# Kernel tuning notes

Hardware: AMD Instinct MI355X
Metric: run time of the kernel (lower is better)

## Reference

```python
import jax, jax.numpy as jnp
import numpy as np

N = 50000      # nodes
DIM = 128      # feature dim
H = 4          # heads
C = DIM // H   # per-head channels
E = 800000     # edges (before self-loops)
LRELU_SLOPE = 0.2
LN_EPS = 1e-5


def setup_inputs() -> dict:
    key = jax.random.key(0)
    ks = jax.random.split(key, 12)
    def p(k, shape, scale=0.05):
        return jax.random.normal(k, shape, jnp.float32) * scale
    return {
        "x": jax.random.normal(ks[0], (N, DIM), jnp.float32),
        "edge_index": jax.random.randint(ks[1], (2, E), 0, N),
        "W1": p(ks[2], (DIM, DIM)), "b1": jnp.zeros((DIM,), jnp.float32),
        "att_src1": p(ks[3], (H, C)), "att_dst1": p(ks[4], (H, C)),
        "W2": p(ks[5], (DIM, DIM)), "b2": jnp.zeros((DIM,), jnp.float32),
        "att_src2": p(ks[6], (H, C)), "att_dst2": p(ks[7], (H, C)),
        "gate_W": p(ks[8], (2 * DIM, 2)), "gate_b": jnp.zeros((2,), jnp.float32),
        "ln_gamma": jnp.ones((DIM,), jnp.float32), "ln_beta": jnp.zeros((DIM,), jnp.float32),
    }


def _gat(x, src, dst, W, b, a_src, a_dst):
    # Linear transform, split heads: [N, H, C]
    h = (x @ W).reshape(-1, H, C)
    # Per-node attention logits per head: [N, H]
    e_src = jnp.einsum("nhc,hc->nh", h, a_src)
    e_dst = jnp.einsum("nhc,hc->nh", h, a_dst)
    # Per-edge logits (edge j->i: src=j, dst=i): [E, H]
    e = jax.nn.leaky_relu(e_src[src] + e_dst[dst], LRELU_SLOPE)
    # Segment softmax over edges sharing a destination (self-loops guarantee >=1 edge/node)
    m = jax.ops.segment_max(e, dst, num_segments=N)
    p = jnp.exp(e - m[dst])
    s = jax.ops.segment_sum(p, dst, num_segments=N)
    alpha = p / s[dst]                                   # [E, H]
    # Weighted scatter-add aggregation
    out = jax.ops.segment_sum(h[src] * alpha[..., None], dst, num_segments=N)
    return out.reshape(-1, H * C) + b                    # [N, DIM]


def reference(x, edge_index, W1, b1, att_src1, att_dst1, W2, b2, att_src2, att_dst2,
              gate_W, gate_b, ln_gamma, ln_beta):
    n = x.shape[0]
    loops = jnp.arange(n, dtype=edge_index.dtype)
    src = jnp.concatenate([edge_index[0], loops])  # PyG GATConv add_self_loops=True
    dst = jnp.concatenate([edge_index[1], loops])
    out1 = _gat(x, src, dst, W1, b1, att_src1, att_dst1)
    out2 = _gat(x, src, dst, W2, b2, att_src2, att_dst2)
    gate = jax.nn.softmax(jnp.concatenate([out1, out2], axis=-1) @ gate_W + gate_b, axis=-1)
    out = gate[:, 0:1] * out1 + gate[:, 1:2] * out2
    # residual + LayerNorm (dropout is identity in eval)
    y = x + out
    mu = jnp.mean(y, axis=-1, keepdims=True)
    var = jnp.var(y, axis=-1, keepdims=True)
    return (y - mu) * jax.lax.rsqrt(var + LN_EPS) * ln_gamma + ln_beta
```

## Files before the change

### kernel.cpp

```cpp
#include <hip/hip_runtime.h>
#include <hip/hip_bf16.h>


typedef unsigned short u16;
typedef __bf16 bf16x8 __attribute__((ext_vector_type(8)));
typedef float f32x4 __attribute__((ext_vector_type(4)));

#define LRELU_SLOPE 0.2f
#define LN_EPS 1e-5f
#define SH 8

__device__ __forceinline__ float bfbits(unsigned int hi_bits) {
    union { unsigned int i; float f; } v; v.i = hi_bits; return v.f;
}
__device__ __forceinline__ float bflo(unsigned int u) { return bfbits(u << 16); }
__device__ __forceinline__ float bfhi(unsigned int u) { return bfbits(u & 0xFFFF0000u); }
__device__ __forceinline__ u16 f2bf(float f) {
    union { float f; unsigned int i; } v; v.f = f;
    unsigned int lsb = (v.i >> 16) & 1u;
    v.i += 0x7FFFu + lsb;
    return (u16)(v.i >> 16);
}

__global__ void k_prep(const float* __restrict__ W1, const float* __restrict__ W2,
                       u16* __restrict__ wb, int* __restrict__ deg8, int n) {
    int i = blockIdx.x * 256 + threadIdx.x;
    if (i < 32768) {
        int col = i >> 7, k = i & 127;
        float v = (col < 128) ? W1[k * 128 + col] : W2[k * 128 + (col - 128)];
        wb[i] = f2bf(v);
    }
    if (i < n) {
#pragma unroll
        for (int x = 0; x < SH; x++) deg8[x * n + i] = 0;
    }
}

__global__ __launch_bounds__(256) void k_cg(const float* __restrict__ x,
                                            const u16* __restrict__ wb,
                                            unsigned int* __restrict__ hbp, int n,
                                            const int* __restrict__ ei,
                                            int* __restrict__ deg8,
                                            int* __restrict__ rnk, int E, int Gg) {
    if ((int)blockIdx.x >= Gg) {
        int i = ((int)blockIdx.x - Gg) * 256 + threadIdx.x;
        if (i < E) {
            int sh = (i >> 8) & (SH - 1);
            int d = ei[E + i];
            rnk[i] = atomicAdd(&deg8[sh * n + d], 1);
        }
        return;
    }
    int wave = threadIdx.x >> 6, lane = threadIdx.x & 63;
    int quad = lane >> 4, r16 = lane & 15;
    int row = blockIdx.x * 64 + wave * 16 + r16;
    int arow = (row < n) ? row : n - 1;
    const float* xp = x + (size_t)arow * 128 + quad * 8;
    union { u16 u[8]; bf16x8 b; } ar;
    bf16x8 a[4];
#pragma unroll
    for (int ks = 0; ks < 4; ks++) {
        float4 lo = *(const float4*)(xp + ks * 32);
        float4 hi = *(const float4*)(xp + ks * 32 + 4);
        ar.u[0] = f2bf(lo.x); ar.u[1] = f2bf(lo.y); ar.u[2] = f2bf(lo.z); ar.u[3] = f2bf(lo.w);
        ar.u[4] = f2bf(hi.x); ar.u[5] = f2bf(hi.y); ar.u[6] = f2bf(hi.z); ar.u[7] = f2bf(hi.w);
        a[ks] = ar.b;
    }
    f32x4 acc[16];
#pragma unroll
    for (int t = 0; t < 16; t++) acc[t] = (f32x4){0.f, 0.f, 0.f, 0.f};
    const u16* bbase = wb + r16 * 128 + quad * 8;
#pragma unroll
    for (int t = 0; t < 16; t++) {
        const u16* bp = bbase + t * 2048;
#pragma unroll
        for (int ks = 0; ks < 4; ks++) {
            bf16x8 b = *(const bf16x8*)(bp + ks * 32);
            acc[t] = __builtin_amdgcn_mfma_f32_16x16x32_bf16(a[ks], b, acc[t], 0, 0, 0);
        }
    }
    int row0 = blockIdx.x * 64 + wave * 16 + quad * 4;
#pragma unroll
    for (int t = 0; t < 8; t++) {
        int c = t * 16 + r16;
#pragma unroll
        for (int g = 0; g < 4; g++) {
            int gr = row0 + g;
            if (gr < n) {
                unsigned int pv = ((unsigned int)f2bf(acc[t + 8][g]) << 16) | f2bf(acc[t][g]);
                hbp[(size_t)gr * 128 + c] = pv;
            }
        }
    }
}

__global__ void k_sb(const int* __restrict__ deg8, int* __restrict__ bsum, int n) {
    __shared__ int s[256];
    int i = blockIdx.x * 256 + threadIdx.x;
    int v = 0;
    if (i < n) {
#pragma unroll
        for (int x = 0; x < SH; x++) v += deg8[x * n + i];
    }
    s[threadIdx.x] = v;
    __syncthreads();
    for (int o = 128; o; o >>= 1) {
        if (threadIdx.x < o) s[threadIdx.x] += s[threadIdx.x + o];
        __syncthreads();
    }
    if (threadIdx.x == 0) bsum[blockIdx.x] = s[0];
}

__global__ void k_scan(int* __restrict__ deg8, const int* __restrict__ bsum,
                       int* __restrict__ offs, int nb, int n) {
    __shared__ int s[256];
    __shared__ int bp;
    int t = threadIdx.x;
    int bv = (t < nb) ? bsum[t] : 0;
    s[t] = bv;
    __syncthreads();
    for (int o = 1; o < 256; o <<= 1) {
        int u = (t >= o) ? s[t - o] : 0;
        __syncthreads();
        s[t] += u;
        __syncthreads();
    }
    if (t == (int)blockIdx.x) bp = s[t] - bv;
    __syncthreads();
    int i = blockIdx.x * 256 + t;
    int d[SH];
    int v = 0;
    if (i < n) {
#pragma unroll
        for (int x = 0; x < SH; x++) { d[x] = deg8[x * n + i]; v += d[x]; }
    }
    s[t] = v;
    __syncthreads();
    for (int o = 1; o < 256; o <<= 1) {
        int u = (t >= o) ? s[t - o] : 0;
        __syncthreads();
        s[t] += u;
        __syncthreads();
    }
    if (i < n) {
        int e = bp + s[t] - v;
        offs[i] = e;
        int run = e;
#pragma unroll
        for (int x = 0; x < SH; x++) { deg8[x * n + i] = run; run += d[x]; }
        if (i == n - 1) offs[n] = e + v;
    }
}

__global__ void k_fl(const int* __restrict__ ei, const int* __restrict__ cursor8,
                     const int* __restrict__ rnk,
                     int* __restrict__ ssrc, int E, int n,
                     const unsigned int* __restrict__ hbp,
                     const float* __restrict__ as1, const float* __restrict__ ad1,
                     const float* __restrict__ as2, const float* __restrict__ ad2,
                     float* __restrict__ es, float* __restrict__ ed, int Gc) {
    if ((int)blockIdx.x >= Gc) {
        int i = ((int)blockIdx.x - Gc) * 256 + threadIdx.x;
        if (i >= n * 4) return;
        int node = i >> 2, head = i & 3;
        const uint4* hv = (const uint4*)(hbp + (size_t)node * 128 + head * 32);
        const float* a1 = as1 + head * 32;
        const float* d1 = ad1 + head * 32;
        const float* a2 = as2 + head * 32;
        const float* d2 = ad2 + head * 32;
        float s1 = 0.f, t1 = 0.f, s2 = 0.f, t2 = 0.f;
#pragma unroll
        for (int q = 0; q < 8; q++) {
            uint4 w = hv[q];
            unsigned int ws[4] = {w.x, w.y, w.z, w.w};
#pragma unroll
            for (int h = 0; h < 4; h++) {
                int c = q * 4 + h;
                float v1 = bflo(ws[h]), v2 = bfhi(ws[h]);
                s1 += v1 * a1[c]; t1 += v1 * d1[c];
                s2 += v2 * a2[c]; t2 += v2 * d2[c];
            }
        }
        *(float2*)(es + node * 8 + head * 2) = make_float2(s1, s2);
        *(float2*)(ed + node * 8 + head * 2) = make_float2(t1, t2);
        return;
    }
    int i = blockIdx.x * 256 + threadIdx.x;
    if (i >= E) return;
    int s = ei[i], d = ei[E + i];
    int sh = (i >> 8) & (SH - 1);
    int pos = cursor8[sh * n + d] + rnk[i];
    ssrc[pos] = s;
}

__device__ __forceinline__ float wred(float v) {
#pragma unroll
    for (int off = 32; off; off >>= 1) v += __shfl_xor(v, off, 64);
    return v;
}

__global__ __launch_bounds__(256) void k_agg(
    const int* __restrict__ offs, const int* __restrict__ ssrc,
    const unsigned int* __restrict__ hbp,
    const float* __restrict__ es, const float* __restrict__ ed,
    const float* __restrict__ b1, const float* __restrict__ b2,
    const float* __restrict__ gW, const float* __restrict__ gb,
    const float* __restrict__ x, const float* __restrict__ gamma,
    const float* __restrict__ beta, float* __restrict__ out, int n) {
    int wave = threadIdx.x >> 6, lane = threadIdx.x & 63;
    int node = blockIdx.x * 4 + wave;
    if (node >= n) return;
    node = __builtin_amdgcn_readfirstlane(node);

    int ca = lane * 2;
    int head = lane >> 4;
    int hh = head * 2;

    float2 edv = *(const float2*)(ed + node * 8 + hh);
    float ed1 = edv.x, ed2 = edv.y;

    float l1 = 0.f, l2 = 0.f;
    float a1a = 0.f, a1b = 0.f, a2a = 0.f, a2b = 0.f;

#define EDGE(sv, q) { \
        float e1 = sv.x + ed1; e1 = fmaxf(e1, LRELU_SLOPE * e1); \
        float e2 = sv.y + ed2; e2 = fmaxf(e2, LRELU_SLOPE * e2); \
        float ww1 = __expf(e1), ww2 = __expf(e2); \
        l1 += ww1; l2 += ww2; \
        a1a += ww1 * bflo(q.x); a1b += ww1 * bflo(q.y); \
        a2a += ww2 * bfhi(q.x); a2b += ww2 * bfhi(q.y); }

    {
        float2 svs = *(const float2*)(es + node * 8 + hh);
        uint2 qs = *(const uint2*)(hbp + (size_t)node * 128 + ca);
        EDGE(svs, qs)
    }

    int beg = offs[node], end = offs[node + 1];
    int k = beg;
    for (; k + 3 < end; k += 4) {
        int j0 = ssrc[k], j1 = ssrc[k + 1], j2 = ssrc[k + 2], j3 = ssrc[k + 3];
        float2 s0 = *(const float2*)(es + j0 * 8 + hh);
        float2 s1 = *(const float2*)(es + j1 * 8 + hh);
        float2 s2 = *(const float2*)(es + j2 * 8 + hh);
        float2 s3 = *(const float2*)(es + j3 * 8 + hh);
        uint2 q0 = *(const uint2*)(hbp + (size_t)j0 * 128 + ca);
        uint2 q1 = *(const uint2*)(hbp + (size_t)j1 * 128 + ca);
        uint2 q2 = *(const uint2*)(hbp + (size_t)j2 * 128 + ca);
        uint2 q3 = *(const uint2*)(hbp + (size_t)j3 * 128 + ca);
        EDGE(s0, q0) EDGE(s1, q1) EDGE(s2, q2) EDGE(s3, q3)
    }
    for (; k < end; k++) {
        int j = ssrc[k];
        float2 sv = *(const float2*)(es + j * 8 + hh);
        uint2 q = *(const uint2*)(hbp + (size_t)j * 128 + ca);
        EDGE(sv, q)
    }
#undef EDGE

    float2 b1v = *(const float2*)(b1 + ca);
    float2 b2v = *(const float2*)(b2 + ca);
    float r1 = 1.f / l1, r2 = 1.f / l2;
    float o1a = a1a * r1 + b1v.x;
    float o1b = a1b * r1 + b1v.y;
    float o2a = a2a * r2 + b2v.x;
    float o2b = a2b * r2 + b2v.y;

    int cb = ca + 1;
    float2 g1a = *(const float2*)(gW + 2 * ca);
    float2 g1b = *(const float2*)(gW + 2 * cb);
    float2 g2a = *(const float2*)(gW + 2 * (128 + ca));
    float2 g2b = *(const float2*)(gW + 2 * (128 + cb));
    float p0 = o1a * g1a.x + o1b * g1b.x + o2a * g2a.x + o2b * g2b.x;
    float p1 = o1a * g1a.y + o1b * g1b.y + o2a * g2a.y + o2b * g2b.y;
    p0 = wred(p0) + gb[0];
    p1 = wred(p1) + gb[1];
    float mg = fmaxf(p0, p1);
    float eg0 = __expf(p0 - mg), eg1 = __expf(p1 - mg);
    float g0 = eg0 / (eg0 + eg1), g1 = 1.f - g0;

    float2 xv = *(const float2*)(x + (size_t)node * 128 + ca);
    float ya = xv.x + g0 * o1a + g1 * o2a;
    float yb = xv.y + g0 * o1b + g1 * o2b;

    float s  = wred(ya + yb);
    float ss = wred(ya * ya + yb * yb);
    float mean = s * (1.f / 128.f);
    float var  = ss * (1.f / 128.f) - mean * mean;
    float rstd = rsqrtf(var + LN_EPS);
    float2 gv = *(const float2*)(gamma + ca);
    float2 bv = *(const float2*)(beta + ca);
    float2 ov;
    ov.x = (ya - mean) * rstd * gv.x + bv.x;
    ov.y = (yb - mean) * rstd * gv.y + bv.y;
    *(float2*)(out + (size_t)node * 128 + ca) = ov;
}

extern "C" void kernel_launch(void* const* d_in, const int* in_sizes, int n_in,
                              void* d_out, int out_size, void* d_ws, size_t ws_size,
                              hipStream_t stream) {
    const float* x   = (const float*)d_in[0];
    const int*   ei  = (const int*)d_in[1];
    const float* W1  = (const float*)d_in[2];
    const float* b1  = (const float*)d_in[3];
    const float* as1 = (const float*)d_in[4];
    const float* ad1 = (const float*)d_in[5];
    const float* W2  = (const float*)d_in[6];
    const float* b2  = (const float*)d_in[7];
    const float* as2 = (const float*)d_in[8];
    const float* ad2 = (const float*)d_in[9];
    const float* gW  = (const float*)d_in[10];
    const float* gb  = (const float*)d_in[11];
    const float* gamma = (const float*)d_in[12];
    const float* beta  = (const float*)d_in[13];
    float* out = (float*)d_out;

    int n = in_sizes[0] / 128;
    int E = in_sizes[1] / 2;

    char* p = (char*)d_ws;
    auto take = [&](size_t bytes) {
        char* q = p;
        p += (bytes + 255) & ~(size_t)255;
        return (void*)q;
    };
    u16* wb    = (u16*)take((size_t)256 * 128 * 2);
    unsigned int* hbp = (unsigned int*)take((size_t)n * 128 * 4);
    float* es  = (float*)take((size_t)n * 8 * 4);
    float* ed  = (float*)take((size_t)n * 8 * 4);
    int* deg8  = (int*)take((size_t)SH * n * 4);
    int* offs  = (int*)take((size_t)(n + 1) * 4);
    int* bsum  = (int*)take((size_t)256 * 4);
    int* ssrc  = (int*)take((size_t)E * 4);
    int* rnk   = (int*)take((size_t)E * 4);

    int nb = (n + 255) / 256;
    int Gg = (n + 63) / 64;
    int Gc = (E + 255) / 256;
    int Gl = (n * 4 + 255) / 256;

    k_prep<<<nb, 256, 0, stream>>>(W1, W2, wb, deg8, n);
    k_cg<<<Gg + Gc, 256, 0, stream>>>(x, wb, hbp, n, ei, deg8, rnk, E, Gg);
    k_sb<<<nb, 256, 0, stream>>>(deg8, bsum, n);
    k_scan<<<nb, 256, 0, stream>>>(deg8, bsum, offs, nb, n);
    k_fl<<<Gc + Gl, 256, 0, stream>>>(ei, deg8, rnk, ssrc, E, n, hbp,
                                      as1, ad1, as2, ad2, es, ed, Gc);
    k_agg<<<(n + 3) / 4, 256, 0, stream>>>(offs, ssrc, hbp, es, ed,
                                           b1, b2, gW, gb, x, gamma, beta, out, n);
}
```

Measured before the change: 260.5 us.

## Stage weights in LDS, fuse scan kernels, pack rank/dst, unroll aggregation

Several changes land together. The weight matrix is pre-swizzled and staged into 64KB of LDS per GEMM block, and each block now covers 128 rows. The two scan kernels are merged into one that uses a global spin barrier over atomics. The edge rank and destination are packed into one word, and the count and fill blocks each handle 4 edges. The aggregation loop is unrolled to 8 edges and the output uses nontemporal stores. Together these aim to cut launch count, memory traffic and latency stalls. The risks are the grid-wide spin barrier, which relies on all 196 blocks being co-resident, reduced occupancy from the 64KB of LDS, and the 17-bit destination packing limit.

```diff
diff --git a/kernel.cpp b/kernel.cpp
--- a/kernel.cpp
+++ b/kernel.cpp
@@ -23,17 +23,23 @@
 }
 
 __global__ void k_prep(const float* __restrict__ W1, const float* __restrict__ W2,
-                       u16* __restrict__ wb, int* __restrict__ deg8, int n) {
+                       u16* __restrict__ wb, int* __restrict__ deg8,
+                       int* __restrict__ gflag, int n) {
     int i = blockIdx.x * 256 + threadIdx.x;
     if (i < 32768) {
-        int col = i >> 7, k = i & 127;
-        float v = (col < 128) ? W1[k * 128 + col] : W2[k * 128 + (col - 128)];
+        int e = i & 7, chunk = i >> 3;
+        int lane = chunk & 63, ks = (chunk >> 6) & 3, t = chunk >> 8;
+        int r16 = lane & 15, quad = lane >> 4;
+        int colp = t * 16 + r16;
+        int k = quad * 8 + ks * 32 + e;
+        float v = (colp < 128) ? W1[k * 128 + colp] : W2[k * 128 + (colp - 128)];
         wb[i] = f2bf(v);
     }
     if (i < n) {
 #pragma unroll
         for (int x = 0; x < SH; x++) deg8[x * n + i] = 0;
     }
+    if (i == 0) *gflag = 0;
 }
 
 __global__ __launch_bounds__(256) void k_cg(const float* __restrict__ x,
@@ -41,92 +47,79 @@
                                             unsigned int* __restrict__ hbp, int n,
                                             const int* __restrict__ ei,
                                             int* __restrict__ deg8,
-                                            int* __restrict__ rnk, int E, int Gg) {
+                                            unsigned int* __restrict__ pk,
+                                            int E, int Gg) {
+    __shared__ u16 lwb[32768];
     if ((int)blockIdx.x >= Gg) {
-        int i = ((int)blockIdx.x - Gg) * 256 + threadIdx.x;
-        if (i < E) {
-            int sh = (i >> 8) & (SH - 1);
-            int d = ei[E + i];
-            rnk[i] = atomicAdd(&deg8[sh * n + d], 1);
+        int bid = (int)blockIdx.x - Gg;
+#pragma unroll
+        for (int it = 0; it < 4; it++) {
+            int i = bid * 1024 + it * 256 + threadIdx.x;
+            if (i < E) {
+                int d = ei[E + i];
+                int sh = (i >> 8) & (SH - 1);
+                unsigned int r = (unsigned int)atomicAdd(&deg8[sh * n + d], 1);
+                pk[i] = (r << 17) | (unsigned int)d;
+            }
         }
         return;
     }
+    {
+        const uint4* g = (const uint4*)wb;
+        uint4* l = (uint4*)lwb;
+#pragma unroll
+        for (int r = 0; r < 16; r++) l[r * 256 + threadIdx.x] = g[r * 256 + threadIdx.x];
+    }
+    __syncthreads();
     int wave = threadIdx.x >> 6, lane = threadIdx.x & 63;
     int quad = lane >> 4, r16 = lane & 15;
-    int row = blockIdx.x * 64 + wave * 16 + r16;
-    int arow = (row < n) ? row : n - 1;
-    const float* xp = x + (size_t)arow * 128 + quad * 8;
-    union { u16 u[8]; bf16x8 b; } ar;
-    bf16x8 a[4];
-#pragma unroll
-    for (int ks = 0; ks < 4; ks++) {
-        float4 lo = *(const float4*)(xp + ks * 32);
-        float4 hi = *(const float4*)(xp + ks * 32 + 4);
-        ar.u[0] = f2bf(lo.x); ar.u[1] = f2bf(lo.y); ar.u[2] = f2bf(lo.z); ar.u[3] = f2bf(lo.w);
-        ar.u[4] = f2bf(hi.x); ar.u[5] = f2bf(hi.y); ar.u[6] = f2bf(hi.z); ar.u[7] = f2bf(hi.w);
-        a[ks] = ar.b;
-    }
-    f32x4 acc[16];
-#pragma unroll
-    for (int t = 0; t < 16; t++) acc[t] = (f32x4){0.f, 0.f, 0.f, 0.f};
-    const u16* bbase = wb + r16 * 128 + quad * 8;
-#pragma unroll
-    for (int t = 0; t < 16; t++) {
-        const u16* bp = bbase + t * 2048;
+    const u16* bb = lwb + lane * 8;
+    for (int strip = 0; strip < 2; strip++) {
+        int row = blockIdx.x * 128 + strip * 64 + wave * 16 + r16;
+        int arow = (row < n) ? row : n - 1;
+        const float* xp = x + (size_t)arow * 128 + quad * 8;
+        union { u16 u[8]; bf16x8 b; } ar;
+        bf16x8 a[4];
 #pragma unroll
         for (int ks = 0; ks < 4; ks++) {
-            bf16x8 b = *(const bf16x8*)(bp + ks * 32);
-            acc[t] = __builtin_amdgcn_mfma_f32_16x16x32_bf16(a[ks], b, acc[t], 0, 0, 0);
-        }
-    }
-    int row0 = blockIdx.x * 64 + wave * 16 + quad * 4;
-#pragma unroll
-    for (int t = 0; t < 8; t++) {
-        int c = t * 16 + r16;
-#pragma unroll
-        for (int g = 0; g < 4; g++) {
-            int gr = row0 + g;
-            if (gr < n) {
-                unsigned int pv = ((unsigned int)f2bf(acc[t + 8][g]) << 16) | f2bf(acc[t][g]);
-                hbp[(size_t)gr * 128 + c] = pv;
+            float4 lo = *(const float4*)(xp + ks * 32);
+            float4 hi = *(const float4*)(xp + ks * 32 + 4);
+            ar.u[0] = f2bf(lo.x); ar.u[1] = f2bf(lo.y); ar.u[2] = f2bf(lo.z); ar.u[3] = f2bf(lo.w);
+            ar.u[4] = f2bf(hi.x); ar.u[5] = f2bf(hi.y); ar.u[6] = f2bf(hi.z); ar.u[7] = f2bf(hi.w);
+            a[ks] = ar.b;
+        }
+        f32x4 acc[16];
+#pragma unroll
+        for (int t = 0; t < 16; t++) acc[t] = (f32x4){0.f, 0.f, 0.f, 0.f};
+#pragma unroll
+        for (int t = 0; t < 16; t++) {
+#pragma unroll
+            for (int ks = 0; ks < 4; ks++) {
+                bf16x8 b = *(const bf16x8*)(bb + (t * 4 + ks) * 512);
+                acc[t] = __builtin_amdgcn_mfma_f32_16x16x32_bf16(a[ks], b, acc[t], 0, 0, 0);
             }
         }
-    }
-}
-
-__global__ void k_sb(const int* __restrict__ deg8, int* __restrict__ bsum, int n) {
+        int row0 = blockIdx.x * 128 + strip * 64 + wave * 16 + quad * 4;
+#pragma unroll
+        for (int t = 0; t < 8; t++) {
+            int c = t * 16 + r16;
+#pragma unroll
+            for (int g = 0; g < 4; g++) {
+                int gr = row0 + g;
+                if (gr < n) {
+                    unsigned int pv = ((unsigned int)f2bf(acc[t + 8][g]) << 16) | f2bf(acc[t][g]);
+                    hbp[(size_t)gr * 128 + c] = pv;
+                }
+            }
+        }
+    }
+}
+
+__global__ void k_ss(int* __restrict__ deg8, int* __restrict__ offs,
+                     int* __restrict__ bsum, int* __restrict__ gflag,
+                     int nb, int n) {
     __shared__ int s[256];
-    int i = blockIdx.x * 256 + threadIdx.x;
-    int v = 0;
-    if (i < n) {
-#pragma unroll
-        for (int x = 0; x < SH; x++) v += deg8[x * n + i];
-    }
-    s[threadIdx.x] = v;
-    __syncthreads();
-    for (int o = 128; o; o >>= 1) {
-        if (threadIdx.x < o) s[threadIdx.x] += s[threadIdx.x + o];
-        __syncthreads();
-    }
-    if (threadIdx.x == 0) bsum[blockIdx.x] = s[0];
-}
-
-__global__ void k_scan(int* __restrict__ deg8, const int* __restrict__ bsum,
-                       int* __restrict__ offs, int nb, int n) {
-    __shared__ int s[256];
-    __shared__ int bp;
     int t = threadIdx.x;
-    int bv = (t < nb) ? bsum[t] : 0;
-    s[t] = bv;
-    __syncthreads();
-    for (int o = 1; o < 256; o <<= 1) {
-        int u = (t >= o) ? s[t - o] : 0;
-        __syncthreads();
-        s[t] += u;
-        __syncthreads();
-    }
-    if (t == (int)blockIdx.x) bp = s[t] - bv;
-    __syncthreads();
     int i = blockIdx.x * 256 + t;
     int d[SH];
     int v = 0;
@@ -142,8 +135,25 @@
         s[t] += u;
         __syncthreads();
     }
+    int myinc = s[t];
+    int total = s[255];
+    if (t == 0) {
+        bsum[blockIdx.x] = total;
+        __threadfence();
+        atomicAdd(gflag, 1);
+        while (atomicAdd(gflag, 0) < nb) { }
+    }
+    __syncthreads();
+    int bv = (t < (int)blockIdx.x) ? atomicAdd(&bsum[t], 0) : 0;
+    s[t] = bv;
+    __syncthreads();
+    for (int o = 128; o; o >>= 1) {
+        if (t < o) s[t] += s[t + o];
+        __syncthreads();
+    }
+    int bp = s[0];
     if (i < n) {
-        int e = bp + s[t] - v;
+        int e = bp + myinc - v;
         offs[i] = e;
         int run = e;
 #pragma unroll
@@ -153,7 +163,7 @@
 }
 
 __global__ void k_fl(const int* __restrict__ ei, const int* __restrict__ cursor8,
-                     const int* __restrict__ rnk,
+                     const unsigned int* __restrict__ pk,
                      int* __restrict__ ssrc, int E, int n,
                      const unsigned int* __restrict__ hbp,
                      const float* __restrict__ as1, const float* __restrict__ ad1,
@@ -185,12 +195,18 @@
         *(float2*)(ed + node * 8 + head * 2) = make_float2(t1, t2);
         return;
     }
-    int i = blockIdx.x * 256 + threadIdx.x;
-    if (i >= E) return;
-    int s = ei[i], d = ei[E + i];
-    int sh = (i >> 8) & (SH - 1);
-    int pos = cursor8[sh * n + d] + rnk[i];
-    ssrc[pos] = s;
+#pragma unroll
+    for (int it = 0; it < 4; it++) {
+        int i = blockIdx.x * 1024 + it * 256 + threadIdx.x;
+        if (i < E) {
+            int s = ei[i];
+            unsigned int v = pk[i];
+            int d = (int)(v & 0x1FFFFu);
+            int r = (int)(v >> 17);
+            int sh = (i >> 8) & (SH - 1);
+            ssrc[cursor8[sh * n + d] + r] = s;
+        }
+    }
 }
 
 __device__ __forceinline__ float wred(float v) {
@@ -238,17 +254,32 @@
 
     int beg = offs[node], end = offs[node + 1];
     int k = beg;
-    for (; k + 3 < end; k += 4) {
-        int j0 = ssrc[k], j1 = ssrc[k + 1], j2 = ssrc[k + 2], j3 = ssrc[k + 3];
-        float2 s0 = *(const float2*)(es + j0 * 8 + hh);
-        float2 s1 = *(const float2*)(es + j1 * 8 + hh);
-        float2 s2 = *(const float2*)(es + j2 * 8 + hh);
-        float2 s3 = *(const float2*)(es + j3 * 8 + hh);
-        uint2 q0 = *(const uint2*)(hbp + (size_t)j0 * 128 + ca);
-        uint2 q1 = *(const uint2*)(hbp + (size_t)j1 * 128 + ca);
-        uint2 q2 = *(const uint2*)(hbp + (size_t)j2 * 128 + ca);
-        uint2 q3 = *(const uint2*)(hbp + (size_t)j3 * 128 + ca);
-        EDGE(s0, q0) EDGE(s1, q1) EDGE(s2, q2) EDGE(s3, q3)
+    for (; k + 7 < end; k += 8) {
+        int jj[8];
+#pragma unroll
+        for (int u = 0; u < 8; u++) jj[u] = ssrc[k + u];
+        float2 sv[8];
+#pragma unroll
+        for (int u = 0; u < 8; u++) sv[u] = *(const float2*)(es + jj[u] * 8 + hh);
+        uint2 qq[8];
+#pragma unroll
+        for (int u = 0; u < 8; u++) qq[u] = *(const uint2*)(hbp + (size_t)jj[u] * 128 + ca);
+#pragma unroll
+        for (int u = 0; u < 8; u++) EDGE(sv[u], qq[u])
+    }
+    if (k + 3 < end) {
+        int jj[4];
+#pragma unroll
+        for (int u = 0; u < 4; u++) jj[u] = ssrc[k + u];
+        float2 sv[4];
+#pragma unroll
+        for (int u = 0; u < 4; u++) sv[u] = *(const float2*)(es + jj[u] * 8 + hh);
+        uint2 qq[4];
+#pragma unroll
+        for (int u = 0; u < 4; u++) qq[u] = *(const uint2*)(hbp + (size_t)jj[u] * 128 + ca);
+#pragma unroll
+        for (int u = 0; u < 4; u++) EDGE(sv[u], qq[u])
+        k += 4;
     }
     for (; k < end; k++) {
         int j = ssrc[k];
@@ -290,10 +321,10 @@
     float rstd = rsqrtf(var + LN_EPS);
     float2 gv = *(const float2*)(gamma + ca);
     float2 bv = *(const float2*)(beta + ca);
-    float2 ov;
-    ov.x = (ya - mean) * rstd * gv.x + bv.x;
-    ov.y = (yb - mean) * rstd * gv.y + bv.y;
-    *(float2*)(out + (size_t)node * 128 + ca) = ov;
+    union { float2 f2; double d; } ov;
+    ov.f2.x = (ya - mean) * rstd * gv.x + bv.x;
+    ov.f2.y = (yb - mean) * rstd * gv.y + bv.y;
+    __builtin_nontemporal_store(ov.d, (double*)(out + (size_t)node * 128 + ca));
 }
 
 extern "C" void kernel_launch(void* const* d_in, const int* in_sizes, int n_in,
@@ -331,20 +362,20 @@
     int* deg8  = (int*)take((size_t)SH * n * 4);
     int* offs  = (int*)take((size_t)(n + 1) * 4);
     int* bsum  = (int*)take((size_t)256 * 4);
+    int* gflag = (int*)take((size_t)256 * 4);
     int* ssrc  = (int*)take((size_t)E * 4);
-    int* rnk   = (int*)take((size_t)E * 4);
-
-    int nb = (n + 255) / 256;
-    int Gg = (n + 63) / 64;
-    int Gc = (E + 255) / 256;
-    int Gl = (n * 4 + 255) / 256;
-
-    k_prep<<<nb, 256, 0, stream>>>(W1, W2, wb, deg8, n);
-    k_cg<<<Gg + Gc, 256, 0, stream>>>(x, wb, hbp, n, ei, deg8, rnk, E, Gg);
-    k_sb<<<nb, 256, 0, stream>>>(deg8, bsum, n);
-    k_scan<<<nb, 256, 0, stream>>>(deg8, bsum, offs, nb, n);
-    k_fl<<<Gc + Gl, 256, 0, stream>>>(ei, deg8, rnk, ssrc, E, n, hbp,
-                                      as1, ad1, as2, ad2, es, ed, Gc);
+    unsigned int* pk = (unsigned int*)take((size_t)E * 4);
+
+    int nb  = (n + 255) / 256;
+    int Gg  = (n + 127) / 128;
+    int Gcc = (E + 1023) / 1024;
+    int Gl  = (n * 4 + 255) / 256;
+
+    k_prep<<<nb, 256, 0, stream>>>(W1, W2, wb, deg8, gflag, n);
+    k_cg<<<Gg + Gcc, 256, 0, stream>>>(x, wb, hbp, n, ei, deg8, pk, E, Gg);
+    k_ss<<<nb, 256, 0, stream>>>(deg8, offs, bsum, gflag, nb, n);
+    k_fl<<<Gcc + Gl, 256, 0, stream>>>(ei, deg8, pk, ssrc, E, n, hbp,
+                                       as1, ad1, as2, ad2, es, ed, Gcc);
     k_agg<<<(n + 3) / 4, 256, 0, stream>>>(offs, ssrc, hbp, es, ed,
                                            b1, b2, gW, gb, x, gamma, beta, out, n);
 }
```

Result: no change. 258.3 us (-0.9%).
